# Performance work log

Measured on AMD Instinct MI355X. Metric: run time of the kernel, lower is better.

The kernel has to match this reference:

```python
import jax, jax.numpy as jnp
import numpy as np

N = 100000   # nodes
E = 1200000  # edges
D = 64       # input_features == hidden_features
L = 3        # num_layers
EPS = 1e-5   # BatchNorm1d eps
SLOPE = 0.2  # LeakyReLU negative slope


def setup_inputs() -> dict:
    key = jax.random.key(0)
    k_x, k_e, k_w = jax.random.split(key, 3)
    x = jax.random.normal(k_x, (N, D), dtype=jnp.float32)
    edge_index = jax.random.randint(k_e, (2, E), 0, N, dtype=jnp.int32)
    # Glorot-ish linear weights per layer, stacked [L, D, D]; bias zeros.
    Ws = jax.random.normal(k_w, (L, D, D), dtype=jnp.float32) / np.float32(np.sqrt(D))
    bs = jnp.zeros((L, D), dtype=jnp.float32)
    # BatchNorm affine params (training-mode batch statistics are used).
    gammas = jnp.ones((L, D), dtype=jnp.float32)
    betas = jnp.zeros((L, D), dtype=jnp.float32)
    return {"x": x, "edge_index": edge_index, "Ws": Ws, "bs": bs,
            "gammas": gammas, "betas": betas}


def reference(x, edge_index, Ws, bs, gammas, betas):
    src, dst = edge_index[0], edge_index[1]
    # GCN symmetric normalization with self-loops: deg = in-degree + 1
    deg = jax.ops.segment_sum(jnp.ones((E,), x.dtype), dst, num_segments=N) + 1.0
    dinv = jax.lax.rsqrt(deg)
    enorm = (dinv[src] * dinv[dst])[:, None]  # [E,1] edge norm
    snorm = (dinv * dinv)[:, None]            # [N,1] self-loop norm
    for l in range(L):
        xw = x @ Ws[l]                                        # [N,D]
        agg = (jax.ops.segment_sum(xw[src] * enorm, dst, num_segments=N)
               + xw * snorm + bs[l])                          # GCNConv output
        h = jnp.where(agg > 0, agg, SLOPE * agg)              # LeakyReLU(0.2)
        mu = h.mean(axis=0)
        var = h.var(axis=0)                                   # biased var (PyTorch BN)
        x = gammas[l] * (h - mu) * jax.lax.rsqrt(var + EPS) + betas[l]
    return x
```

## Files before the change

### kernel.cpp

```cpp
#include <hip/hip_runtime.h>

#define D 64
#define SLOPE 0.2f
#define BN_EPS 1e-5f
#define BSHIFT 9
#define BUCKET 512
#define CHUNK 8192

static __device__ __forceinline__ unsigned pk_bf16(float fx, float fy) {
    unsigned bx = __float_as_uint(fx);
    unsigned by = __float_as_uint(fy);
    bx = (bx + 0x7fffu + ((bx >> 16) & 1u)) >> 16;
    by = (by + 0x7fffu + ((by >> 16) & 1u)) & 0xffff0000u;
    return bx | by;
}
static __device__ __forceinline__ float bf_lo(unsigned u) { return __uint_as_float(u << 16); }
static __device__ __forceinline__ float bf_hi(unsigned u) { return __uint_as_float(u & 0xffff0000u); }

__global__ __launch_bounds__(256) void k_hist(const int* __restrict__ dst,
                                              int* __restrict__ bcnt, int E) {
    __shared__ int hist[256];
    hist[threadIdx.x] = 0;
    __syncthreads();
    for (int e = blockIdx.x * 256 + threadIdx.x; e < E; e += gridDim.x * 256)
        atomicAdd(&hist[dst[e] >> BSHIFT], 1);
    __syncthreads();
    const int v = hist[threadIdx.x];
    if (v) atomicAdd(&bcnt[threadIdx.x], v);
}

__global__ __launch_bounds__(256) void k_bscan(const int* __restrict__ bcnt,
                                               int* __restrict__ bbase, int* __restrict__ pcur,
                                               unsigned* __restrict__ ybf, int NB, int E, int N) {
    __shared__ int l[256];
    const int t = threadIdx.x;
    const int v = (t < NB) ? bcnt[t] : 0;
    l[t] = v;
    __syncthreads();
    for (int off = 1; off < 256; off <<= 1) {
        int x = l[t];
        if (t >= off) x += l[t - off];
        __syncthreads();
        l[t] = x;
        __syncthreads();
    }
    const int excl = l[t] - v;
    if (t < NB) { bbase[t] = excl; pcur[t] = excl; }
    if (t == 0) bbase[NB] = E;
    if (t < 32) ybf[(size_t)N * 32 + t] = 0u;
}

__global__ __launch_bounds__(256) void k_part(const int* __restrict__ src,
                                              const int* __restrict__ dst,
                                              int* __restrict__ pcur,
                                              unsigned* __restrict__ arena, int E) {
    __shared__ unsigned stage[CHUNK];
    __shared__ unsigned char bktb[CHUNK];
    __shared__ int hist[256], lofs[256], gbase[256];
    const int t = threadIdx.x;
    const int e0 = blockIdx.x * CHUNK;
    const int cn = min(CHUNK, E - e0);

    hist[t] = 0;
    __syncthreads();
    for (int i = t; i < cn; i += 256)
        atomicAdd(&hist[dst[e0 + i] >> BSHIFT], 1);
    __syncthreads();
    const int v = hist[t];
    lofs[t] = v;
    __syncthreads();
    for (int off = 1; off < 256; off <<= 1) {
        int x = lofs[t];
        if (t >= off) x += lofs[t - off];
        __syncthreads();
        lofs[t] = x;
        __syncthreads();
    }
    const int excl = lofs[t] - v;
    __syncthreads();
    lofs[t] = excl;
    if (v > 0) gbase[t] = atomicAdd(&pcur[t], v);
    __syncthreads();
    for (int i = t; i < cn; i += 256) {
        const int dd = dst[e0 + i];
        const int b  = dd >> BSHIFT;
        const int p  = atomicAdd(&lofs[b], 1);
        stage[p] = ((unsigned)(dd & (BUCKET - 1)) << 23) | (unsigned)src[e0 + i];
        bktb[p]  = (unsigned char)b;
    }
    __syncthreads();
    for (int i = t; i < cn; i += 256) {
        const int b = bktb[i];
        const int startb = lofs[b] - hist[b];
        arena[gbase[b] + (i - startb)] = stage[i];
    }
}

__global__ __launch_bounds__(512) void k_build(const unsigned* __restrict__ arena,
                                               const int* __restrict__ bbase,
                                               int* __restrict__ rp, int* __restrict__ pcnt,
                                               int* __restrict__ colbuf, float* __restrict__ dinv,
                                               int N) {
    __shared__ int ncnt[512], sc[512], lcur[512];
    const int t = threadIdx.x;
    const int nbase  = blockIdx.x << BSHIFT;
    const int nlocal = min(BUCKET, N - nbase);
    const int abeg = bbase[blockIdx.x];
    const int aend = bbase[blockIdx.x + 1];
    const int pbase = abeg + 7 * nbase;

    ncnt[t] = 0;
    __syncthreads();
    for (int i = abeg + t; i < aend; i += 512)
        atomicAdd(&ncnt[arena[i] >> 23], 1);
    __syncthreads();
    const int v = ncnt[t];
    const int p = (v + 7) & ~7;
    sc[t] = p;
    __syncthreads();
    for (int off = 1; off < 512; off <<= 1) {
        int x = sc[t];
        if (t >= off) x += sc[t - off];
        __syncthreads();
        sc[t] = x;
        __syncthreads();
    }
    const int excl = sc[t] - p;
    lcur[t] = pbase + excl;
    if (t < nlocal) {
        rp[nbase + t]   = pbase + excl;
        pcnt[nbase + t] = p;
        dinv[nbase + t] = rsqrtf((float)v + 1.0f);
    }
    __syncthreads();
    for (int i = abeg + t; i < aend; i += 512) {
        const unsigned u = arena[i];
        const int pos = atomicAdd(&lcur[u >> 23], 1);
        colbuf[pos] = (int)(u & 0x7FFFFFu);
    }
    if (t < nlocal)
        for (int k = v; k < p; ++k) colbuf[pbase + excl + k] = N;
}

__global__ __launch_bounds__(256) void k_gemm(const float* __restrict__ x,
                                              const float* __restrict__ W,
                                              const float* __restrict__ stats,
                                              const float* __restrict__ gamma,
                                              const float* __restrict__ beta,
                                              const float* __restrict__ dinv,
                                              unsigned* __restrict__ ybf,
                                              float invN, int affine, int N) {
    __shared__ float scs[D], shs[D];
    const int tid = threadIdx.x;
    if (tid < D) {
        float sc = 1.f, sh = 0.f;
        if (affine) {
            const float mu  = stats[tid] * invN;
            const float var = stats[D + tid] * invN - mu * mu;
            sc = gamma[tid] * rsqrtf(var + BN_EPS);
            sh = beta[tid] - mu * sc;
        }
        scs[tid] = sc; shs[tid] = sh;
    }
    __syncthreads();

    const int lane = tid & 63;
    const int wib  = tid >> 6;
    float Wreg[D];
    float bv = 0.f;
#pragma unroll
    for (int k = 0; k < D; ++k) {
        const float w = W[k * D + lane];
        Wreg[k] = scs[k] * w;
        bv = fmaf(shs[k], w, bv);
    }
    const int stride = gridDim.x * 4;
    for (int row = __builtin_amdgcn_readfirstlane(blockIdx.x * 4 + wib); row < N; row += stride) {
        const float4* xr = (const float4*)(x + (size_t)row * D);
        float acc = 0.f;
#pragma unroll
        for (int k4 = 0; k4 < 16; ++k4) {
            const float4 xv = xr[k4];
            acc = fmaf(xv.x, Wreg[4 * k4 + 0], acc);
            acc = fmaf(xv.y, Wreg[4 * k4 + 1], acc);
            acc = fmaf(xv.z, Wreg[4 * k4 + 2], acc);
            acc = fmaf(xv.w, Wreg[4 * k4 + 3], acc);
        }
        const float r  = (acc + bv) * dinv[row];
        const float rn = __shfl_down(r, 1, 64);
        if (!(lane & 1))
            ybf[(size_t)row * 32 + (lane >> 1)] = pk_bf16(r, rn);
    }
}

__global__ __launch_bounds__(256) void k_pull(const int* __restrict__ rp,
                                              const int* __restrict__ pcnt,
                                              const int* __restrict__ colbuf,
                                              const unsigned* __restrict__ ybf,
                                              const float* __restrict__ dinv,
                                              const float* __restrict__ b,
                                              float* __restrict__ h,
                                              float* __restrict__ stats, int N) {
    const int tid  = threadIdx.x;
    const int lane = tid & 63;
    const int t32  = lane & 31;
    const int hw   = lane >> 5;
    const int wv   = tid >> 6;
    const float b0 = b[2 * t32];
    const float b1 = b[2 * t32 + 1];
    float s1a = 0.f, s1b = 0.f, s2a = 0.f, s2b = 0.f;

    const int gw = blockIdx.x * 4 + wv;
    const int gstride = gridDim.x * 4;

    for (int pr = gw; 2 * pr < N; pr += gstride) {
        const int n  = 2 * pr + hw;
        const bool vn = n < N;
        const int st = vn ? rp[n]   : 0;
        const int pd = vn ? pcnt[n] : 0;

        float a[8][2];
#pragma unroll
        for (int c = 0; c < 8; ++c) { a[c][0] = 0.f; a[c][1] = 0.f; }
        {
            const unsigned u = vn ? ybf[(size_t)n * 32 + t32] : 0u;
            a[0][0] = bf_lo(u); a[0][1] = bf_hi(u);
        }
        for (int w0 = 0; w0 < pd; w0 += 32) {
            const int wn = min(pd - w0, 32);
            const int ci = (t32 < wn) ? colbuf[st + w0 + t32] : 0;
            for (int j0 = 0; j0 < wn; j0 += 8) {
#pragma unroll
                for (int jj = 0; jj < 8; ++jj) {
                    const int idx = __shfl(ci, hw * 32 + j0 + jj, 64);
                    const unsigned u = ybf[(size_t)idx * 32 + t32];
                    a[jj][0] += bf_lo(u);
                    a[jj][1] += bf_hi(u);
                }
            }
        }
        const float v0 = ((a[0][0] + a[1][0]) + (a[2][0] + a[3][0])) +
                         ((a[4][0] + a[5][0]) + (a[6][0] + a[7][0]));
        const float v1 = ((a[0][1] + a[1][1]) + (a[2][1] + a[3][1])) +
                         ((a[4][1] + a[5][1]) + (a[6][1] + a[7][1]));
        if (vn) {
            const float di = dinv[n];
            float t0 = fmaf(di, v0, b0); t0 = t0 > 0.f ? t0 : SLOPE * t0;
            float t1 = fmaf(di, v1, b1); t1 = t1 > 0.f ? t1 : SLOPE * t1;
            *(float2*)&h[(size_t)n * D + 2 * t32] = make_float2(t0, t1);
            s1a += t0; s2a += t0 * t0;
            s1b += t1; s2b += t1 * t1;
        }
    }

    __shared__ float l1[64], l2[64];
    if (tid < 64) { l1[tid] = 0.f; l2[tid] = 0.f; }
    __syncthreads();
    atomicAdd(&l1[2 * t32],     s1a);
    atomicAdd(&l1[2 * t32 + 1], s1b);
    atomicAdd(&l2[2 * t32],     s2a);
    atomicAdd(&l2[2 * t32 + 1], s2b);
    __syncthreads();
    if (tid < 64) {
        atomicAdd(&stats[tid],      l1[tid]);
        atomicAdd(&stats[64 + tid], l2[tid]);
    }
}

__global__ __launch_bounds__(256) void k_normalize(const float* __restrict__ h,
                                                   const float* __restrict__ stats,
                                                   const float* __restrict__ gamma,
                                                   const float* __restrict__ beta,
                                                   float* __restrict__ out,
                                                   float invN, int total4) {
    const int gt = blockIdx.x * 256 + threadIdx.x;
    const int c0 = (gt * 4) & 63;
    float sc[4], sh[4];
#pragma unroll
    for (int k = 0; k < 4; ++k) {
        const int c = c0 + k;
        const float mu  = stats[c] * invN;
        const float var = stats[64 + c] * invN - mu * mu;
        sc[k] = gamma[c] * rsqrtf(var + BN_EPS);
        sh[k] = beta[c] - mu * sc[k];
    }
    const float4* h4 = (const float4*)h;
    float4* o4 = (float4*)out;
    for (int i = gt; i < total4; i += gridDim.x * 256) {
        float4 v = h4[i];
        v.x = fmaf(sc[0], v.x, sh[0]);
        v.y = fmaf(sc[1], v.y, sh[1]);
        v.z = fmaf(sc[2], v.z, sh[2]);
        v.w = fmaf(sc[3], v.w, sh[3]);
        o4[i] = v;
    }
}

extern "C" void kernel_launch(void* const* d_in, const int* in_sizes, int n_in,
                              void* d_out, int out_size, void* d_ws, size_t ws_size,
                              hipStream_t stream) {
    const float* x0     = (const float*)d_in[0];
    const int*   ei     = (const int*)d_in[1];
    const float* Ws     = (const float*)d_in[2];
    const float* bs     = (const float*)d_in[3];
    const float* gammas = (const float*)d_in[4];
    const float* betas  = (const float*)d_in[5];

    const int N = in_sizes[0] / D;
    const int E = in_sizes[1] / 2;
    const int L = in_sizes[2] / (D * D);
    const int NB = (N + BUCKET - 1) >> BSHIFT;
    const int nchunks = (E + CHUNK - 1) / CHUNK;

    const int* srcp = ei;
    const int* dstp = ei + E;

    char* wsb = (char*)d_ws;
    size_t o = 0;
    auto alloc = [&](size_t elems) { size_t r = o; o += (elems + 255) & ~(size_t)255; return r; };
    const size_t o_bcnt  = alloc(256);
    const size_t o_stats = alloc((size_t)L * 128);
    const size_t zero_end = o;
    const size_t o_bbase = alloc(257);
    const size_t o_pcur  = alloc(256);
    const size_t o_rp    = alloc((size_t)N);
    const size_t o_pcnt  = alloc((size_t)N);
    const size_t o_dinv  = alloc((size_t)N);
    const size_t o_arena = alloc((size_t)E);
    const size_t o_col   = alloc((size_t)E + 7 * (size_t)N + 64);
    const size_t o_y     = alloc(((size_t)N + 1) * 32);
    const size_t o_h     = alloc((size_t)N * D);

    int*      bcnt  = (int*)(wsb + o_bcnt * 4);
    float*    stats = (float*)(wsb + o_stats * 4);
    int*      bbase = (int*)(wsb + o_bbase * 4);
    int*      pcur  = (int*)(wsb + o_pcur * 4);
    int*      rp    = (int*)(wsb + o_rp * 4);
    int*      pcnt  = (int*)(wsb + o_pcnt * 4);
    float*    dinv  = (float*)(wsb + o_dinv * 4);
    unsigned* arena = (unsigned*)(wsb + o_arena * 4);
    int*      col   = (int*)(wsb + o_col * 4);
    unsigned* ybf   = (unsigned*)(wsb + o_y * 4);
    float*    h     = (float*)(wsb + o_h * 4);
    float*    out   = (float*)d_out;

    hipMemsetAsync(d_ws, 0, zero_end * 4, stream);

    k_hist <<<512, 256, 0, stream>>>(dstp, bcnt, E);
    k_bscan<<<1,   256, 0, stream>>>(bcnt, bbase, pcur, ybf, NB, E, N);
    k_part <<<nchunks, 256, 0, stream>>>(srcp, dstp, pcur, arena, E);
    k_build<<<NB,  512, 0, stream>>>(arena, bbase, rp, pcnt, col, dinv, N);

    const float invN = 1.0f / (float)N;
    const float* xin = x0;
    for (int l = 0; l < L; ++l) {
        const int pl = l ? l - 1 : 0;
        k_gemm<<<1024, 256, 0, stream>>>(xin, Ws + (size_t)l * D * D,
                                         stats + (size_t)pl * 128,
                                         gammas + (size_t)pl * D, betas + (size_t)pl * D,
                                         dinv, ybf, invN, l > 0 ? 1 : 0, N);
        k_pull<<<2048, 256, 0, stream>>>(rp, pcnt, col, ybf, dinv, bs + (size_t)l * D,
                                         h, stats + (size_t)l * 128, N);
        xin = h;
    }
    k_normalize<<<1024, 256, 0, stream>>>(h, stats + (size_t)(L - 1) * 128,
                                          gammas + (size_t)(L - 1) * D,
                                          betas + (size_t)(L - 1) * D,
                                          out, invN, N * D / 4);
}
```

Baseline: 407.3 us.

## Fuse layer loop into one persistent cooperative kernel with grid syncs

```diff
diff --git a/kernel.cpp b/kernel.cpp
--- a/kernel.cpp
+++ b/kernel.cpp
@@ -1,4 +1,7 @@
 #include <hip/hip_runtime.h>
+#include <hip/hip_cooperative_groups.h>
+
+namespace cg = cooperative_groups;
 
 #define D 64
 #define SLOPE 0.2f
@@ -140,6 +143,157 @@
     }
     if (t < nlocal)
         for (int k = v; k < p; ++k) colbuf[pbase + excl + k] = N;
+}
+
+__global__ __launch_bounds__(256, 4) void k_layers(
+    const float* __restrict__ x0, const float* __restrict__ Ws, const float* __restrict__ bs,
+    const float* __restrict__ gammas, const float* __restrict__ betas,
+    const int* __restrict__ rp, const int* __restrict__ pcnt, const int* __restrict__ colbuf,
+    const float* __restrict__ dinv, unsigned* __restrict__ ybf,
+    float* __restrict__ h, float* __restrict__ stats, float* __restrict__ out,
+    float invN, int N, int L)
+{
+    cg::grid_group grid = cg::this_grid();
+    __shared__ float scs[D], shs[D], l1[D], l2[D];
+    const int tid  = threadIdx.x;
+    const int bid  = blockIdx.x;
+    const int lane = tid & 63;
+    const int wv   = tid >> 6;
+    const int t32  = lane & 31;
+    const int hw   = lane >> 5;
+    const int nwaves = gridDim.x * 4;
+    const int gwave  = bid * 4 + wv;
+
+    for (int l = 0; l < L; ++l) {
+        if (tid < D) {
+            float sc = 1.f, sh = 0.f;
+            if (l > 0) {
+                const float* st = stats + (size_t)(l - 1) * 128;
+                const float mu  = st[tid] * invN;
+                const float var = st[D + tid] * invN - mu * mu;
+                sc = gammas[(l - 1) * D + tid] * rsqrtf(var + BN_EPS);
+                sh = betas[(l - 1) * D + tid] - mu * sc;
+            }
+            scs[tid] = sc; shs[tid] = sh;
+        }
+        __syncthreads();
+
+        {
+            const float* Wl = Ws + (size_t)l * D * D;
+            float Wreg[D];
+            float bv = 0.f;
+#pragma unroll
+            for (int k = 0; k < D; ++k) {
+                const float w = Wl[k * D + lane];
+                Wreg[k] = scs[k] * w;
+                bv = fmaf(shs[k], w, bv);
+            }
+            const float* xin = (l == 0) ? x0 : h;
+            for (int row = __builtin_amdgcn_readfirstlane(gwave); row < N; row += nwaves) {
+                const float4* xr = (const float4*)(xin + (size_t)row * D);
+                float acc = 0.f;
+#pragma unroll
+                for (int k4 = 0; k4 < 16; ++k4) {
+                    const float4 xv = xr[k4];
+                    acc = fmaf(xv.x, Wreg[4 * k4 + 0], acc);
+                    acc = fmaf(xv.y, Wreg[4 * k4 + 1], acc);
+                    acc = fmaf(xv.z, Wreg[4 * k4 + 2], acc);
+                    acc = fmaf(xv.w, Wreg[4 * k4 + 3], acc);
+                }
+                const float r  = (acc + bv) * dinv[row];
+                const float rn = __shfl_down(r, 1, 64);
+                if (!(lane & 1))
+                    ybf[(size_t)row * 32 + (lane >> 1)] = pk_bf16(r, rn);
+            }
+        }
+        grid.sync();
+
+        {
+            const float b0 = bs[l * D + 2 * t32];
+            const float b1 = bs[l * D + 2 * t32 + 1];
+            float s1a = 0.f, s1b = 0.f, s2a = 0.f, s2b = 0.f;
+
+            for (int pr = gwave; 2 * pr < N; pr += nwaves) {
+                const int n  = 2 * pr + hw;
+                const bool vn = n < N;
+                const int st = vn ? rp[n]   : 0;
+                const int pd = vn ? pcnt[n] : 0;
+
+                float a[8][2];
+#pragma unroll
+                for (int c = 0; c < 8; ++c) { a[c][0] = 0.f; a[c][1] = 0.f; }
+                {
+                    const unsigned u = vn ? ybf[(size_t)n * 32 + t32] : 0u;
+                    a[0][0] = bf_lo(u); a[0][1] = bf_hi(u);
+                }
+                for (int w0 = 0; w0 < pd; w0 += 32) {
+                    const int wn = min(pd - w0, 32);
+                    const int ci = (t32 < wn) ? colbuf[st + w0 + t32] : 0;
+                    for (int j0 = 0; j0 < wn; j0 += 8) {
+#pragma unroll
+                        for (int jj = 0; jj < 8; ++jj) {
+                            const int idx = __shfl(ci, hw * 32 + j0 + jj, 64);
+                            const unsigned u = ybf[(size_t)idx * 32 + t32];
+                            a[jj][0] += bf_lo(u);
+                            a[jj][1] += bf_hi(u);
+                        }
+                    }
+                }
+                const float v0 = ((a[0][0] + a[1][0]) + (a[2][0] + a[3][0])) +
+                                 ((a[4][0] + a[5][0]) + (a[6][0] + a[7][0]));
+                const float v1 = ((a[0][1] + a[1][1]) + (a[2][1] + a[3][1])) +
+                                 ((a[4][1] + a[5][1]) + (a[6][1] + a[7][1]));
+                if (vn) {
+                    const float di = dinv[n];
+                    float t0 = fmaf(di, v0, b0); t0 = t0 > 0.f ? t0 : SLOPE * t0;
+                    float t1 = fmaf(di, v1, b1); t1 = t1 > 0.f ? t1 : SLOPE * t1;
+                    *(float2*)&h[(size_t)n * D + 2 * t32] = make_float2(t0, t1);
+                    s1a += t0; s2a += t0 * t0;
+                    s1b += t1; s2b += t1 * t1;
+                }
+            }
+
+            if (tid < D) { l1[tid] = 0.f; l2[tid] = 0.f; }
+            __syncthreads();
+            atomicAdd(&l1[2 * t32],     s1a);
+            atomicAdd(&l1[2 * t32 + 1], s1b);
+            atomicAdd(&l2[2 * t32],     s2a);
+            atomicAdd(&l2[2 * t32 + 1], s2b);
+            __syncthreads();
+            if (tid < D) {
+                float* stl = stats + (size_t)l * 128;
+                atomicAdd(&stl[tid],     l1[tid]);
+                atomicAdd(&stl[D + tid], l2[tid]);
+            }
+        }
+        grid.sync();
+    }
+
+    {
+        const float* st = stats + (size_t)(L - 1) * 128;
+        const int gt = bid * 256 + tid;
+        const int c0 = (gt * 4) & 63;
+        float sc[4], sh[4];
+#pragma unroll
+        for (int k = 0; k < 4; ++k) {
+            const int c = c0 + k;
+            const float mu  = st[c] * invN;
+            const float var = st[D + c] * invN - mu * mu;
+            sc[k] = gammas[(L - 1) * D + c] * rsqrtf(var + BN_EPS);
+            sh[k] = betas[(L - 1) * D + c] - mu * sc[k];
+        }
+        const int total4 = N * D / 4;
+        const float4* h4 = (const float4*)h;
+        float4* o4 = (float4*)out;
+        for (int i = gt; i < total4; i += gridDim.x * 256) {
+            float4 v = h4[i];
+            v.x = fmaf(sc[0], v.x, sh[0]);
+            v.y = fmaf(sc[1], v.y, sh[1]);
+            v.z = fmaf(sc[2], v.z, sh[2]);
+            v.w = fmaf(sc[3], v.w, sh[3]);
+            o4[i] = v;
+        }
+    }
 }
 
 __global__ __launch_bounds__(256) void k_gemm(const float* __restrict__ x,
@@ -163,7 +317,6 @@
         scs[tid] = sc; shs[tid] = sh;
     }
     __syncthreads();
-
     const int lane = tid & 63;
     const int wib  = tid >> 6;
     float Wreg[D];
@@ -209,7 +362,6 @@
     const float b0 = b[2 * t32];
     const float b1 = b[2 * t32 + 1];
     float s1a = 0.f, s1b = 0.f, s2a = 0.f, s2b = 0.f;
-
     const int gw = blockIdx.x * 4 + wv;
     const int gstride = gridDim.x * 4;
 
@@ -218,7 +370,6 @@
         const bool vn = n < N;
         const int st = vn ? rp[n]   : 0;
         const int pd = vn ? pcnt[n] : 0;
-
         float a[8][2];
 #pragma unroll
         for (int c = 0; c < 8; ++c) { a[c][0] = 0.f; a[c][1] = 0.f; }
@@ -252,7 +403,6 @@
             s1b += t1; s2b += t1 * t1;
         }
     }
-
     __shared__ float l1[64], l2[64];
     if (tid < 64) { l1[tid] = 0.f; l2[tid] = 0.f; }
     __syncthreads();
@@ -352,19 +502,41 @@
     k_build<<<NB,  512, 0, stream>>>(arena, bbase, rp, pcnt, col, dinv, N);
 
     const float invN = 1.0f / (float)N;
-    const float* xin = x0;
-    for (int l = 0; l < L; ++l) {
-        const int pl = l ? l - 1 : 0;
-        k_gemm<<<1024, 256, 0, stream>>>(xin, Ws + (size_t)l * D * D,
-                                         stats + (size_t)pl * 128,
-                                         gammas + (size_t)pl * D, betas + (size_t)pl * D,
-                                         dinv, ybf, invN, l > 0 ? 1 : 0, N);
-        k_pull<<<2048, 256, 0, stream>>>(rp, pcnt, col, ybf, dinv, bs + (size_t)l * D,
-                                         h, stats + (size_t)l * 128, N);
-        xin = h;
-    }
-    k_normalize<<<1024, 256, 0, stream>>>(h, stats + (size_t)(L - 1) * 128,
-                                          gammas + (size_t)(L - 1) * D,
-                                          betas + (size_t)(L - 1) * D,
-                                          out, invN, N * D / 4);
-}
+
+    int dev = 0, nCU = 0, maxB = 0;
+    bool coop = (hipGetDevice(&dev) == hipSuccess)
+             && (hipDeviceGetAttribute(&nCU, hipDeviceAttributeMultiprocessorCount, dev) == hipSuccess)
+             && (hipOccupancyMaxActiveBlocksPerMultiprocessor(&maxB, (const void*)k_layers, 256, 0) == hipSuccess)
+             && nCU > 0 && maxB > 0;
+    if (coop) {
+        int gridsz = nCU * maxB;
+        float invN_a = invN;
+        int N_a = N, L_a = L;
+        void* args[] = {
+            (void*)&x0, (void*)&Ws, (void*)&bs, (void*)&gammas, (void*)&betas,
+            (void*)&rp, (void*)&pcnt, (void*)&col, (void*)&dinv, (void*)&ybf,
+            (void*)&h, (void*)&stats, (void*)&out,
+            (void*)&invN_a, (void*)&N_a, (void*)&L_a
+        };
+        coop = hipLaunchCooperativeKernel((void*)k_layers, dim3(gridsz), dim3(256),
+                                          args, 0, stream) == hipSuccess;
+    }
+    if (!coop) {
+        (void)hipGetLastError();
+        const float* xin = x0;
+        for (int l = 0; l < L; ++l) {
+            const int pl = l ? l - 1 : 0;
+            k_gemm<<<1024, 256, 0, stream>>>(xin, Ws + (size_t)l * D * D,
+                                             stats + (size_t)pl * 128,
+                                             gammas + (size_t)pl * D, betas + (size_t)pl * D,
+                                             dinv, ybf, invN, l > 0 ? 1 : 0, N);
+            k_pull<<<2048, 256, 0, stream>>>(rp, pcnt, col, ybf, dinv, bs + (size_t)l * D,
+                                             h, stats + (size_t)l * 128, N);
+            xin = h;
+        }
+        k_normalize<<<1024, 256, 0, stream>>>(h, stats + (size_t)(L - 1) * 128,
+                                              gammas + (size_t)(L - 1) * D,
+                                              betas + (size_t)(L - 1) * D,
+                                              out, invN, N * D / 4);
+    }
+}
```

Measured after the change: 779.9 us. 91.5% more time.

## Rework pull aggregation to 16-lane rows with 4 edges per wave step

Applied to the files above, without the earlier changes.

```diff
diff --git a/kernel.cpp b/kernel.cpp
--- a/kernel.cpp
+++ b/kernel.cpp
@@ -18,10 +18,12 @@
 static __device__ __forceinline__ float bf_hi(unsigned u) { return __uint_as_float(u & 0xffff0000u); }
 
 __global__ __launch_bounds__(256) void k_hist(const int* __restrict__ dst,
-                                              int* __restrict__ bcnt, int E) {
+                                              int* __restrict__ bcnt,
+                                              unsigned* __restrict__ ybf, int E, int N) {
     __shared__ int hist[256];
     hist[threadIdx.x] = 0;
     __syncthreads();
+    if (blockIdx.x == 0 && threadIdx.x < 32) ybf[(size_t)N * 32 + threadIdx.x] = 0u;
     for (int e = blockIdx.x * 256 + threadIdx.x; e < E; e += gridDim.x * 256)
         atomicAdd(&hist[dst[e] >> BSHIFT], 1);
     __syncthreads();
@@ -29,40 +31,34 @@
     if (v) atomicAdd(&bcnt[threadIdx.x], v);
 }
 
-__global__ __launch_bounds__(256) void k_bscan(const int* __restrict__ bcnt,
-                                               int* __restrict__ bbase, int* __restrict__ pcur,
-                                               unsigned* __restrict__ ybf, int NB, int E, int N) {
-    __shared__ int l[256];
-    const int t = threadIdx.x;
-    const int v = (t < NB) ? bcnt[t] : 0;
-    l[t] = v;
-    __syncthreads();
-    for (int off = 1; off < 256; off <<= 1) {
-        int x = l[t];
-        if (t >= off) x += l[t - off];
-        __syncthreads();
-        l[t] = x;
-        __syncthreads();
-    }
-    const int excl = l[t] - v;
-    if (t < NB) { bbase[t] = excl; pcur[t] = excl; }
-    if (t == 0) bbase[NB] = E;
-    if (t < 32) ybf[(size_t)N * 32 + t] = 0u;
-}
-
 __global__ __launch_bounds__(256) void k_part(const int* __restrict__ src,
                                               const int* __restrict__ dst,
+                                              const int* __restrict__ bcnt,
                                               int* __restrict__ pcur,
                                               unsigned* __restrict__ arena, int E) {
     __shared__ unsigned stage[CHUNK];
     __shared__ unsigned char bktb[CHUNK];
-    __shared__ int hist[256], lofs[256], gbase[256];
+    __shared__ int bscan[256], hist[256], lofs[256], gbase[256];
     const int t = threadIdx.x;
     const int e0 = blockIdx.x * CHUNK;
     const int cn = min(CHUNK, E - e0);
 
+    const int bv = bcnt[t];
+    bscan[t] = bv;
+    __syncthreads();
+    for (int off = 1; off < 256; off <<= 1) {
+        int x = bscan[t];
+        if (t >= off) x += bscan[t - off];
+        __syncthreads();
+        bscan[t] = x;
+        __syncthreads();
+    }
+    const int bexcl = bscan[t] - bv;
+    __syncthreads();
+    bscan[t] = bexcl;
     hist[t] = 0;
     __syncthreads();
+
     for (int i = t; i < cn; i += 256)
         atomicAdd(&hist[dst[e0 + i] >> BSHIFT], 1);
     __syncthreads();
@@ -79,7 +75,7 @@
     const int excl = lofs[t] - v;
     __syncthreads();
     lofs[t] = excl;
-    if (v > 0) gbase[t] = atomicAdd(&pcur[t], v);
+    if (v > 0) gbase[t] = bscan[t] + atomicAdd(&pcur[t], v);
     __syncthreads();
     for (int i = t; i < cn; i += 256) {
         const int dd = dst[e0 + i];
@@ -97,17 +93,34 @@
 }
 
 __global__ __launch_bounds__(512) void k_build(const unsigned* __restrict__ arena,
-                                               const int* __restrict__ bbase,
+                                               const int* __restrict__ bcnt,
                                                int* __restrict__ rp, int* __restrict__ pcnt,
                                                int* __restrict__ colbuf, float* __restrict__ dinv,
-                                               int N) {
-    __shared__ int ncnt[512], sc[512], lcur[512];
+                                               int N, int E) {
+    __shared__ int bscan[257], ncnt[512], sc[512], lcur[512];
     const int t = threadIdx.x;
-    const int nbase  = blockIdx.x << BSHIFT;
+    if (t < 256) { bscan[t] = bcnt[t]; }
+    __syncthreads();
+    if (t < 256) {
+        for (int off = 1; off < 256; off <<= 1) {
+            int x = bscan[t];
+            if (t >= off) x += bscan[t - off];
+            __syncthreads();
+            bscan[t] = x;
+            __syncthreads();
+        }
+    } else {
+        for (int off = 1; off < 256; off <<= 1) { __syncthreads(); __syncthreads(); }
+    }
+    if (t == 0) bscan[256] = 0;
+    __syncthreads();
+
+    const int b = blockIdx.x;
+    const int nbase  = b << BSHIFT;
     const int nlocal = min(BUCKET, N - nbase);
-    const int abeg = bbase[blockIdx.x];
-    const int aend = bbase[blockIdx.x + 1];
-    const int pbase = abeg + 7 * nbase;
+    const int abeg = (b == 0) ? 0 : bscan[b - 1];
+    const int aend = bscan[b];
+    const int pbase = (abeg + 15 * nbase + 15) & ~15;
 
     ncnt[t] = 0;
     __syncthreads();
@@ -115,7 +128,7 @@
         atomicAdd(&ncnt[arena[i] >> 23], 1);
     __syncthreads();
     const int v = ncnt[t];
-    const int p = (v + 7) & ~7;
+    const int p = (v + 15) & ~15;
     sc[t] = p;
     __syncthreads();
     for (int off = 1; off < 512; off <<= 1) {
@@ -163,7 +176,6 @@
         scs[tid] = sc; shs[tid] = sh;
     }
     __syncthreads();
-
     const int lane = tid & 63;
     const int wib  = tid >> 6;
     float Wreg[D];
@@ -196,74 +208,125 @@
 __global__ __launch_bounds__(256) void k_pull(const int* __restrict__ rp,
                                               const int* __restrict__ pcnt,
                                               const int* __restrict__ colbuf,
-                                              const unsigned* __restrict__ ybf,
+                                              const uint2* __restrict__ ybf2,
                                               const float* __restrict__ dinv,
                                               const float* __restrict__ b,
                                               float* __restrict__ h,
                                               float* __restrict__ stats, int N) {
     const int tid  = threadIdx.x;
     const int lane = tid & 63;
-    const int t32  = lane & 31;
-    const int hw   = lane >> 5;
+    const int sl   = lane & 15;
+    const int e4   = lane >> 4;
     const int wv   = tid >> 6;
-    const float b0 = b[2 * t32];
-    const float b1 = b[2 * t32 + 1];
-    float s1a = 0.f, s1b = 0.f, s2a = 0.f, s2b = 0.f;
+    float bb[4];
+#pragma unroll
+    for (int f = 0; f < 4; ++f) bb[f] = b[4 * sl + f];
+    float s1k[4] = {0.f, 0.f, 0.f, 0.f}, s2k[4] = {0.f, 0.f, 0.f, 0.f};
 
     const int gw = blockIdx.x * 4 + wv;
     const int gstride = gridDim.x * 4;
 
     for (int pr = gw; 2 * pr < N; pr += gstride) {
-        const int n  = 2 * pr + hw;
-        const bool vn = n < N;
-        const int st = vn ? rp[n]   : 0;
-        const int pd = vn ? pcnt[n] : 0;
-
-        float a[8][2];
-#pragma unroll
-        for (int c = 0; c < 8; ++c) { a[c][0] = 0.f; a[c][1] = 0.f; }
-        {
-            const unsigned u = vn ? ybf[(size_t)n * 32 + t32] : 0u;
-            a[0][0] = bf_lo(u); a[0][1] = bf_hi(u);
-        }
-        for (int w0 = 0; w0 < pd; w0 += 32) {
-            const int wn = min(pd - w0, 32);
-            const int ci = (t32 < wn) ? colbuf[st + w0 + t32] : 0;
-            for (int j0 = 0; j0 < wn; j0 += 8) {
-#pragma unroll
-                for (int jj = 0; jj < 8; ++jj) {
-                    const int idx = __shfl(ci, hw * 32 + j0 + jj, 64);
-                    const unsigned u = ybf[(size_t)idx * 32 + t32];
-                    a[jj][0] += bf_lo(u);
-                    a[jj][1] += bf_hi(u);
+        const int pru = __builtin_amdgcn_readfirstlane(pr);
+        const int nA = 2 * pru;
+        const int nB = nA + 1;
+        const bool hasB = nB < N;
+        const int stA = __builtin_amdgcn_readfirstlane(rp[nA]);
+        const int pdA = __builtin_amdgcn_readfirstlane(pcnt[nA]);
+        int stB = 0, pdB = 0;
+        if (hasB) {
+            stB = __builtin_amdgcn_readfirstlane(rp[nB]);
+            pdB = __builtin_amdgcn_readfirstlane(pcnt[nB]);
+        }
+
+        float accA[4][4], accB[4][4];
+#pragma unroll
+        for (int c = 0; c < 4; ++c)
+#pragma unroll
+            for (int f = 0; f < 4; ++f) { accA[c][f] = 0.f; accB[c][f] = 0.f; }
+
+        for (int g = 0; g < pdA; g += 16) {
+#pragma unroll
+            for (int c = 0; c < 4; ++c) {
+                const int4 ip = *(const int4*)&colbuf[stA + g + 4 * c];
+                int id = ip.x;
+                id = (e4 == 1) ? ip.y : id;
+                id = (e4 == 2) ? ip.z : id;
+                id = (e4 == 3) ? ip.w : id;
+                const uint2 u = ybf2[(size_t)id * 16 + sl];
+                accA[c][0] += bf_lo(u.x); accA[c][1] += bf_hi(u.x);
+                accA[c][2] += bf_lo(u.y); accA[c][3] += bf_hi(u.y);
+            }
+        }
+        for (int g = 0; g < pdB; g += 16) {
+#pragma unroll
+            for (int c = 0; c < 4; ++c) {
+                const int4 ip = *(const int4*)&colbuf[stB + g + 4 * c];
+                int id = ip.x;
+                id = (e4 == 1) ? ip.y : id;
+                id = (e4 == 2) ? ip.z : id;
+                id = (e4 == 3) ? ip.w : id;
+                const uint2 u = ybf2[(size_t)id * 16 + sl];
+                accB[c][0] += bf_lo(u.x); accB[c][1] += bf_hi(u.x);
+                accB[c][2] += bf_lo(u.y); accB[c][3] += bf_hi(u.y);
+            }
+        }
+
+        float vA[4], vB[4];
+#pragma unroll
+        for (int f = 0; f < 4; ++f) {
+            vA[f] = (accA[0][f] + accA[1][f]) + (accA[2][f] + accA[3][f]);
+            vA[f] += __shfl_xor(vA[f], 16, 64);
+            vA[f] += __shfl_xor(vA[f], 32, 64);
+            vB[f] = (accB[0][f] + accB[1][f]) + (accB[2][f] + accB[3][f]);
+            vB[f] += __shfl_xor(vB[f], 16, 64);
+            vB[f] += __shfl_xor(vB[f], 32, 64);
+        }
+
+        if (lane < 16) {
+            {
+                const uint2 su = ybf2[(size_t)nA * 16 + sl];
+                const float self[4] = {bf_lo(su.x), bf_hi(su.x), bf_lo(su.y), bf_hi(su.y)};
+                const float di = dinv[nA];
+                float4 hv; float* hp = &hv.x;
+#pragma unroll
+                for (int f = 0; f < 4; ++f) {
+                    float t = fmaf(di, vA[f] + self[f], bb[f]);
+                    t = t > 0.f ? t : SLOPE * t;
+                    hp[f] = t; s1k[f] += t; s2k[f] += t * t;
                 }
+                *(float4*)&h[(size_t)nA * D + 4 * sl] = hv;
             }
-        }
-        const float v0 = ((a[0][0] + a[1][0]) + (a[2][0] + a[3][0])) +
-                         ((a[4][0] + a[5][0]) + (a[6][0] + a[7][0]));
-        const float v1 = ((a[0][1] + a[1][1]) + (a[2][1] + a[3][1])) +
-                         ((a[4][1] + a[5][1]) + (a[6][1] + a[7][1]));
-        if (vn) {
-            const float di = dinv[n];
-            float t0 = fmaf(di, v0, b0); t0 = t0 > 0.f ? t0 : SLOPE * t0;
-            float t1 = fmaf(di, v1, b1); t1 = t1 > 0.f ? t1 : SLOPE * t1;
-            *(float2*)&h[(size_t)n * D + 2 * t32] = make_float2(t0, t1);
-            s1a += t0; s2a += t0 * t0;
-            s1b += t1; s2b += t1 * t1;
-        }
-    }
-
-    __shared__ float l1[64], l2[64];
-    if (tid < 64) { l1[tid] = 0.f; l2[tid] = 0.f; }
-    __syncthreads();
-    atomicAdd(&l1[2 * t32],     s1a);
-    atomicAdd(&l1[2 * t32 + 1], s1b);
-    atomicAdd(&l2[2 * t32],     s2a);
-    atomicAdd(&l2[2 * t32 + 1], s2b);
+            if (hasB) {
+                const uint2 su = ybf2[(size_t)nB * 16 + sl];
+                const float self[4] = {bf_lo(su.x), bf_hi(su.x), bf_lo(su.y), bf_hi(su.y)};
+                const float di = dinv[nB];
+                float4 hv; float* hp = &hv.x;
+#pragma unroll
+                for (int f = 0; f < 4; ++f) {
+                    float t = fmaf(di, vB[f] + self[f], bb[f]);
+                    t = t > 0.f ? t : SLOPE * t;
+                    hp[f] = t; s1k[f] += t; s2k[f] += t * t;
+                }
+                *(float4*)&h[(size_t)nB * D + 4 * sl] = hv;
+            }
+        }
+    }
+
+    __shared__ float ls1[64], ls2[64];
+    if (tid < 64) { ls1[tid] = 0.f; ls2[tid] = 0.f; }
+    __syncthreads();
+    if (lane < 16) {
+#pragma unroll
+        for (int f = 0; f < 4; ++f) {
+            atomicAdd(&ls1[4 * sl + f], s1k[f]);
+            atomicAdd(&ls2[4 * sl + f], s2k[f]);
+        }
+    }
     __syncthreads();
     if (tid < 64) {
-        atomicAdd(&stats[tid],      l1[tid]);
-        atomicAdd(&stats[64 + tid], l2[tid]);
+        atomicAdd(&stats[tid],      ls1[tid]);
+        atomicAdd(&stats[64 + tid], ls2[tid]);
     }
 }
 
@@ -309,8 +372,8 @@
     const int N = in_sizes[0] / D;
     const int E = in_sizes[1] / 2;
     const int L = in_sizes[2] / (D * D);
+    const int nchunks = (E + CHUNK - 1) / CHUNK;
     const int NB = (N + BUCKET - 1) >> BSHIFT;
-    const int nchunks = (E + CHUNK - 1) / CHUNK;
 
     const int* srcp = ei;
     const int* dstp = ei + E;
@@ -319,22 +382,20 @@
     size_t o = 0;
     auto alloc = [&](size_t elems) { size_t r = o; o += (elems + 255) & ~(size_t)255; return r; };
     const size_t o_bcnt  = alloc(256);
+    const size_t o_pcur  = alloc(256);
     const size_t o_stats = alloc((size_t)L * 128);
     const size_t zero_end = o;
-    const size_t o_bbase = alloc(257);
-    const size_t o_pcur  = alloc(256);
     const size_t o_rp    = alloc((size_t)N);
     const size_t o_pcnt  = alloc((size_t)N);
     const size_t o_dinv  = alloc((size_t)N);
     const size_t o_arena = alloc((size_t)E);
-    const size_t o_col   = alloc((size_t)E + 7 * (size_t)N + 64);
+    const size_t o_col   = alloc((size_t)E + 15 * (size_t)N + 16 * 256 + 256);
     const size_t o_y     = alloc(((size_t)N + 1) * 32);
     const size_t o_h     = alloc((size_t)N * D);
 
     int*      bcnt  = (int*)(wsb + o_bcnt * 4);
+    int*      pcur  = (int*)(wsb + o_pcur * 4);
     float*    stats = (float*)(wsb + o_stats * 4);
-    int*      bbase = (int*)(wsb + o_bbase * 4);
-    int*      pcur  = (int*)(wsb + o_pcur * 4);
     int*      rp    = (int*)(wsb + o_rp * 4);
     int*      pcnt  = (int*)(wsb + o_pcnt * 4);
     float*    dinv  = (float*)(wsb + o_dinv * 4);
@@ -346,10 +407,9 @@
 
     hipMemsetAsync(d_ws, 0, zero_end * 4, stream);
 
-    k_hist <<<512, 256, 0, stream>>>(dstp, bcnt, E);
-    k_bscan<<<1,   256, 0, stream>>>(bcnt, bbase, pcur, ybf, NB, E, N);
-    k_part <<<nchunks, 256, 0, stream>>>(srcp, dstp, pcur, arena, E);
-    k_build<<<NB,  512, 0, stream>>>(arena, bbase, rp, pcnt, col, dinv, N);
+    k_hist <<<512, 256, 0, stream>>>(dstp, bcnt, ybf, E, N);
+    k_part <<<nchunks, 256, 0, stream>>>(srcp, dstp, bcnt, pcur, arena, E);
+    k_build<<<NB, 512, 0, stream>>>(arena, bcnt, rp, pcnt, col, dinv, N, E);
 
     const float invN = 1.0f / (float)N;
     const float* xin = x0;
@@ -359,8 +419,8 @@
                                          stats + (size_t)pl * 128,
                                          gammas + (size_t)pl * D, betas + (size_t)pl * D,
                                          dinv, ybf, invN, l > 0 ? 1 : 0, N);
-        k_pull<<<2048, 256, 0, stream>>>(rp, pcnt, col, ybf, dinv, bs + (size_t)l * D,
-                                         h, stats + (size_t)l * 128, N);
+        k_pull<<<2048, 256, 0, stream>>>(rp, pcnt, col, (const uint2*)ybf, dinv,
+                                         bs + (size_t)l * D, h, stats + (size_t)l * 128, N);
         xin = h;
     }
     k_normalize<<<1024, 256, 0, stream>>>(h, stats + (size_t)(L - 1) * 128,
```

After: 425.6 us. 1.04x slower.

## Degree-sort nodes within buckets for pull load balance and drop bucket-scan kernel

Applied to the files above, without the earlier changes.

```diff
diff --git a/kernel.cpp b/kernel.cpp
--- a/kernel.cpp
+++ b/kernel.cpp
@@ -18,10 +18,12 @@
 static __device__ __forceinline__ float bf_hi(unsigned u) { return __uint_as_float(u & 0xffff0000u); }
 
 __global__ __launch_bounds__(256) void k_hist(const int* __restrict__ dst,
-                                              int* __restrict__ bcnt, int E) {
+                                              int* __restrict__ bcnt,
+                                              unsigned* __restrict__ ybf, int E, int N) {
     __shared__ int hist[256];
     hist[threadIdx.x] = 0;
     __syncthreads();
+    if (blockIdx.x == 0 && threadIdx.x < 32) ybf[(size_t)N * 32 + threadIdx.x] = 0u;
     for (int e = blockIdx.x * 256 + threadIdx.x; e < E; e += gridDim.x * 256)
         atomicAdd(&hist[dst[e] >> BSHIFT], 1);
     __syncthreads();
@@ -29,40 +31,34 @@
     if (v) atomicAdd(&bcnt[threadIdx.x], v);
 }
 
-__global__ __launch_bounds__(256) void k_bscan(const int* __restrict__ bcnt,
-                                               int* __restrict__ bbase, int* __restrict__ pcur,
-                                               unsigned* __restrict__ ybf, int NB, int E, int N) {
-    __shared__ int l[256];
-    const int t = threadIdx.x;
-    const int v = (t < NB) ? bcnt[t] : 0;
-    l[t] = v;
-    __syncthreads();
-    for (int off = 1; off < 256; off <<= 1) {
-        int x = l[t];
-        if (t >= off) x += l[t - off];
-        __syncthreads();
-        l[t] = x;
-        __syncthreads();
-    }
-    const int excl = l[t] - v;
-    if (t < NB) { bbase[t] = excl; pcur[t] = excl; }
-    if (t == 0) bbase[NB] = E;
-    if (t < 32) ybf[(size_t)N * 32 + t] = 0u;
-}
-
 __global__ __launch_bounds__(256) void k_part(const int* __restrict__ src,
                                               const int* __restrict__ dst,
+                                              const int* __restrict__ bcnt,
                                               int* __restrict__ pcur,
                                               unsigned* __restrict__ arena, int E) {
     __shared__ unsigned stage[CHUNK];
     __shared__ unsigned char bktb[CHUNK];
-    __shared__ int hist[256], lofs[256], gbase[256];
+    __shared__ int bscan[256], hist[256], lofs[256], gbase[256];
     const int t = threadIdx.x;
     const int e0 = blockIdx.x * CHUNK;
     const int cn = min(CHUNK, E - e0);
 
+    const int bv = bcnt[t];
+    bscan[t] = bv;
+    __syncthreads();
+    for (int off = 1; off < 256; off <<= 1) {
+        int x = bscan[t];
+        if (t >= off) x += bscan[t - off];
+        __syncthreads();
+        bscan[t] = x;
+        __syncthreads();
+    }
+    const int bexcl = bscan[t] - bv;
+    __syncthreads();
+    bscan[t] = bexcl;
     hist[t] = 0;
     __syncthreads();
+
     for (int i = t; i < cn; i += 256)
         atomicAdd(&hist[dst[e0 + i] >> BSHIFT], 1);
     __syncthreads();
@@ -79,7 +75,7 @@
     const int excl = lofs[t] - v;
     __syncthreads();
     lofs[t] = excl;
-    if (v > 0) gbase[t] = atomicAdd(&pcur[t], v);
+    if (v > 0) gbase[t] = bscan[t] + atomicAdd(&pcur[t], v);
     __syncthreads();
     for (int i = t; i < cn; i += 256) {
         const int dd = dst[e0 + i];
@@ -97,16 +93,32 @@
 }
 
 __global__ __launch_bounds__(512) void k_build(const unsigned* __restrict__ arena,
-                                               const int* __restrict__ bbase,
+                                               const int* __restrict__ bcnt,
                                                int* __restrict__ rp, int* __restrict__ pcnt,
                                                int* __restrict__ colbuf, float* __restrict__ dinv,
-                                               int N) {
-    __shared__ int ncnt[512], sc[512], lcur[512];
+                                               int* __restrict__ perm, int N) {
+    __shared__ int bscan[256], ncnt[512], sc[512], lcur[512];
     const int t = threadIdx.x;
-    const int nbase  = blockIdx.x << BSHIFT;
+    if (t < 256) bscan[t] = bcnt[t];
+    __syncthreads();
+    if (t < 256) {
+        for (int off = 1; off < 256; off <<= 1) {
+            int x = bscan[t];
+            if (t >= off) x += bscan[t - off];
+            __syncthreads();
+            bscan[t] = x;
+            __syncthreads();
+        }
+    } else {
+        for (int off = 1; off < 256; off <<= 1) { __syncthreads(); __syncthreads(); }
+    }
+    __syncthreads();
+
+    const int b = blockIdx.x;
+    const int nbase  = b << BSHIFT;
     const int nlocal = min(BUCKET, N - nbase);
-    const int abeg = bbase[blockIdx.x];
-    const int aend = bbase[blockIdx.x + 1];
+    const int abeg = (b == 0) ? 0 : bscan[b - 1];
+    const int aend = bscan[b];
     const int pbase = abeg + 7 * nbase;
 
     ncnt[t] = 0;
@@ -140,6 +152,31 @@
     }
     if (t < nlocal)
         for (int k = v; k < p; ++k) colbuf[pbase + excl + k] = N;
+
+    __syncthreads();
+    const int dkey = v > 511 ? 511 : v;
+    ncnt[t] = 0;
+    lcur[t] = 0;
+    __syncthreads();
+    if (t < nlocal) atomicAdd(&ncnt[dkey], 1);
+    __syncthreads();
+    sc[t] = ncnt[t];
+    __syncthreads();
+    for (int off = 1; off < 512; off <<= 1) {
+        int x = sc[t];
+        if (t >= off) x += sc[t - off];
+        __syncthreads();
+        sc[t] = x;
+        __syncthreads();
+    }
+    __syncthreads();
+    if (t < nlocal) {
+        const int binstart = sc[dkey] - ncnt[dkey];
+        const int rank = atomicAdd(&lcur[dkey], 1);
+        perm[nbase + binstart + rank] = nbase + t;
+    } else {
+        perm[nbase + t] = -1;
+    }
 }
 
 __global__ __launch_bounds__(256) void k_gemm(const float* __restrict__ x,
@@ -163,7 +200,6 @@
         scs[tid] = sc; shs[tid] = sh;
     }
     __syncthreads();
-
     const int lane = tid & 63;
     const int wib  = tid >> 6;
     float Wreg[D];
@@ -199,8 +235,10 @@
                                               const unsigned* __restrict__ ybf,
                                               const float* __restrict__ dinv,
                                               const float* __restrict__ b,
+                                              const int* __restrict__ perm,
                                               float* __restrict__ h,
-                                              float* __restrict__ stats, int N) {
+                                              float* __restrict__ stats,
+                                              int npairs, int N) {
     const int tid  = threadIdx.x;
     const int lane = tid & 63;
     const int t32  = lane & 31;
@@ -209,13 +247,12 @@
     const float b0 = b[2 * t32];
     const float b1 = b[2 * t32 + 1];
     float s1a = 0.f, s1b = 0.f, s2a = 0.f, s2b = 0.f;
-
     const int gw = blockIdx.x * 4 + wv;
     const int gstride = gridDim.x * 4;
 
-    for (int pr = gw; 2 * pr < N; pr += gstride) {
-        const int n  = 2 * pr + hw;
-        const bool vn = n < N;
+    for (int pr = gw; pr < npairs; pr += gstride) {
+        const int n  = perm[2 * pr + hw];
+        const bool vn = n >= 0;
         const int st = vn ? rp[n]   : 0;
         const int pd = vn ? pcnt[n] : 0;
 
@@ -309,8 +346,9 @@
     const int N = in_sizes[0] / D;
     const int E = in_sizes[1] / 2;
     const int L = in_sizes[2] / (D * D);
+    const int nchunks = (E + CHUNK - 1) / CHUNK;
     const int NB = (N + BUCKET - 1) >> BSHIFT;
-    const int nchunks = (E + CHUNK - 1) / CHUNK;
+    const int npairs = NB * (BUCKET / 2);
 
     const int* srcp = ei;
     const int* dstp = ei + E;
@@ -319,25 +357,25 @@
     size_t o = 0;
     auto alloc = [&](size_t elems) { size_t r = o; o += (elems + 255) & ~(size_t)255; return r; };
     const size_t o_bcnt  = alloc(256);
+    const size_t o_pcur  = alloc(256);
     const size_t o_stats = alloc((size_t)L * 128);
     const size_t zero_end = o;
-    const size_t o_bbase = alloc(257);
-    const size_t o_pcur  = alloc(256);
     const size_t o_rp    = alloc((size_t)N);
     const size_t o_pcnt  = alloc((size_t)N);
     const size_t o_dinv  = alloc((size_t)N);
+    const size_t o_perm  = alloc((size_t)NB * BUCKET);
     const size_t o_arena = alloc((size_t)E);
-    const size_t o_col   = alloc((size_t)E + 7 * (size_t)N + 64);
+    const size_t o_col   = alloc((size_t)E + 7 * (size_t)N + 512);
     const size_t o_y     = alloc(((size_t)N + 1) * 32);
     const size_t o_h     = alloc((size_t)N * D);
 
     int*      bcnt  = (int*)(wsb + o_bcnt * 4);
+    int*      pcur  = (int*)(wsb + o_pcur * 4);
     float*    stats = (float*)(wsb + o_stats * 4);
-    int*      bbase = (int*)(wsb + o_bbase * 4);
-    int*      pcur  = (int*)(wsb + o_pcur * 4);
     int*      rp    = (int*)(wsb + o_rp * 4);
     int*      pcnt  = (int*)(wsb + o_pcnt * 4);
     float*    dinv  = (float*)(wsb + o_dinv * 4);
+    int*      perm  = (int*)(wsb + o_perm * 4);
     unsigned* arena = (unsigned*)(wsb + o_arena * 4);
     int*      col   = (int*)(wsb + o_col * 4);
     unsigned* ybf   = (unsigned*)(wsb + o_y * 4);
@@ -346,10 +384,9 @@
 
     hipMemsetAsync(d_ws, 0, zero_end * 4, stream);
 
-    k_hist <<<512, 256, 0, stream>>>(dstp, bcnt, E);
-    k_bscan<<<1,   256, 0, stream>>>(bcnt, bbase, pcur, ybf, NB, E, N);
-    k_part <<<nchunks, 256, 0, stream>>>(srcp, dstp, pcur, arena, E);
-    k_build<<<NB,  512, 0, stream>>>(arena, bbase, rp, pcnt, col, dinv, N);
+    k_hist <<<512, 256, 0, stream>>>(dstp, bcnt, ybf, E, N);
+    k_part <<<nchunks, 256, 0, stream>>>(srcp, dstp, bcnt, pcur, arena, E);
+    k_build<<<NB, 512, 0, stream>>>(arena, bcnt, rp, pcnt, col, dinv, perm, N);
 
     const float invN = 1.0f / (float)N;
     const float* xin = x0;
@@ -359,8 +396,9 @@
                                          stats + (size_t)pl * 128,
                                          gammas + (size_t)pl * D, betas + (size_t)pl * D,
                                          dinv, ybf, invN, l > 0 ? 1 : 0, N);
-        k_pull<<<2048, 256, 0, stream>>>(rp, pcnt, col, ybf, dinv, bs + (size_t)l * D,
-                                         h, stats + (size_t)l * 128, N);
+        k_pull<<<2048, 256, 0, stream>>>(rp, pcnt, col, ybf, dinv,
+                                         bs + (size_t)l * D, perm, h,
+                                         stats + (size_t)l * 128, npairs, N);
         xin = h;
     }
     k_normalize<<<1024, 256, 0, stream>>>(h, stats + (size_t)(L - 1) * 128,
```

After: 425.6 us. +4.5%, slower.
